# Kernel tuning notes

Hardware: AMD Instinct MI355X
Metric: run time of the kernel (lower is better)

Reference implementation:

```python
import jax, jax.numpy as jnp
import numpy as np

N_NODES = 50000
N_EDGES = 800000
IN_CH = 256
HID = 64
HEADS = 4
NEG_SLOPE = 0.2  # PyG GATConv default


def setup_inputs() -> dict:
    key = jax.random.key(0)
    ks = jax.random.split(key, 12)
    glorot = lambda k, shape: jax.random.normal(k, shape, jnp.float32) * (2.0 / (shape[0] + shape[-1])) ** 0.5
    d1 = HEADS * HID  # 256: width after conv1 (concat heads)
    return {
        "x": jax.random.normal(ks[0], (N_NODES, IN_CH), jnp.float32),
        "edge_index": jax.random.randint(ks[1], (2, N_EDGES), 0, N_NODES, jnp.int64),
        # conv1: GATConv(IN_CH, HID, heads=HEADS)
        "W1": glorot(ks[2], (IN_CH, HEADS * HID)),
        "a_src1": glorot(ks[3], (HEADS, HID)),
        "a_dst1": glorot(ks[4], (HEADS, HID)),
        "b1": jnp.zeros((HEADS * HID,), jnp.float32),
        # conv2: GATConv(d1, d1, heads=1)
        "W2": glorot(ks[5], (d1, d1)),
        "a_src2": glorot(ks[6], (1, d1)),
        "a_dst2": glorot(ks[7], (1, d1)),
        "b2": jnp.zeros((d1,), jnp.float32),
    }


def gat_conv(x, src, dst, W, a_src, a_dst, b, heads, out_ch, n_nodes):
    """PyG-style GATConv: per-head linear, additive attention, segment softmax over dst."""
    h = (x @ W).reshape(n_nodes, heads, out_ch)            # [N, H, C]
    alpha_src = jnp.sum(h * a_src, axis=-1)                # [N, H]
    alpha_dst = jnp.sum(h * a_dst, axis=-1)                # [N, H]
    e = jax.nn.leaky_relu(alpha_src[src] + alpha_dst[dst], NEG_SLOPE)  # [E, H]
    # numerically-stable segment softmax grouped by destination node
    e_max = jax.ops.segment_max(e, dst, num_segments=n_nodes)         # [N, H]
    e_exp = jnp.exp(e - e_max[dst])
    denom = jax.ops.segment_sum(e_exp, dst, num_segments=n_nodes)
    alpha = e_exp / denom[dst]                                        # [E, H]
    out = jax.ops.segment_sum(alpha[:, :, None] * h[src], dst, num_segments=n_nodes)  # [N, H, C]
    return out.reshape(n_nodes, heads * out_ch) + b


def reference(x, edge_index, W1, a_src1, a_dst1, b1, W2, a_src2, a_dst2, b2):
    n = x.shape[0]
    loops = jnp.arange(n, dtype=edge_index.dtype)
    src = jnp.concatenate([edge_index[0], loops])  # add self-loops (PyG default)
    dst = jnp.concatenate([edge_index[1], loops])
    h1 = gat_conv(x, src, dst, W1, a_src1, a_dst1, b1, HEADS, HID, n)
    h1 = jax.nn.elu(h1)
    out = gat_conv(h1, src, dst, W2, a_src2, a_dst2, b2, 1, HEADS * HID, n)
    return out
```

## Files before the change

kernel.cpp:

```cpp
#include <hip/hip_runtime.h>
#include <stdint.h>

typedef __bf16 bfv8 __attribute__((ext_vector_type(8)));
typedef float f32x4 __attribute__((ext_vector_type(4)));

__device__ __forceinline__ float b2f(unsigned short u) {
    union { unsigned int i; float f; } v; v.i = ((unsigned int)u) << 16; return v.f;
}
__device__ __forceinline__ unsigned short f2b(float f) {
    unsigned int x = __float_as_uint(f);
    unsigned int r = x + 0x7FFFu + ((x >> 16) & 1u);
    return (unsigned short)(r >> 16);
}
__device__ __forceinline__ float squash(float v) {
    return (v == v && fabsf(v) < 1e30f) ? v : 0.f;
}
__device__ __forceinline__ float blo(unsigned int w) {
    union { unsigned int i; float f; } v; v.i = w << 16; return v.f;
}
__device__ __forceinline__ float bhi(unsigned int w) {
    union { unsigned int i; float f; } v; v.i = w & 0xffff0000u; return v.f;
}

__device__ __forceinline__ void detect_reg(const void* x, const void* ei, int& f32w, int& i64w) {
    const unsigned short* xu = (const unsigned short*)x;
    const int* e32 = (const int*)ei;
    int bad = 0, oz = 0;
#pragma unroll
    for (int j = 0; j < 64; j++) {
        float v = b2f(xu[j]);
        if (!(fabsf(v) < 1e10f)) bad++;
    }
#pragma unroll
    for (int j = 1; j < 16; j += 2)
        if (e32[j] == 0) oz++;
    f32w = (bad >= 2) ? 1 : 0;
    i64w = (oz >= 6) ? 1 : 0;
}

__device__ __forceinline__ int edge_at(const void* ei, int idx, int i64) {
    return i64 ? (int)(((const long long*)ei)[idx]) : ((const int*)ei)[idx];
}

__global__ __launch_bounds__(256) void k_prep(
        const void* __restrict__ x, const void* __restrict__ ei,
        const void* __restrict__ W1, const void* __restrict__ W2,
        const void* __restrict__ a_src1, const void* __restrict__ a_dst1, const void* __restrict__ b1,
        const void* __restrict__ a_src2, const void* __restrict__ a_dst2, const void* __restrict__ b2,
        unsigned short* __restrict__ xb, unsigned short* __restrict__ WT1,
        unsigned short* __restrict__ WT2, unsigned short* __restrict__ vecs,
        int* __restrict__ deg, int* __restrict__ flags,
        int E, int ET, int N, int total8, int nconv, int nhist) {
    __shared__ unsigned short t[32][33];
    int f32w, i64w;
    detect_reg(x, ei, f32w, i64w);
    int b = blockIdx.x;
    int tid = threadIdx.x;

    if (b < nconv) {
        int i = b * 256 + tid;
        if (i >= total8) return;
        if (f32w) {
            const float4* f = (const float4*)x;
            float4 a = f[2 * i], bb = f[2 * i + 1];
            uint4 o;
            o.x = (unsigned)f2b(squash(a.x)) | ((unsigned)f2b(squash(a.y)) << 16);
            o.y = (unsigned)f2b(squash(a.z)) | ((unsigned)f2b(squash(a.w)) << 16);
            o.z = (unsigned)f2b(squash(bb.x)) | ((unsigned)f2b(squash(bb.y)) << 16);
            o.w = (unsigned)f2b(squash(bb.z)) | ((unsigned)f2b(squash(bb.w)) << 16);
            *(uint4*)(xb + 8 * (size_t)i) = o;
        } else {
            *(uint4*)(xb + 8 * (size_t)i) = ((const uint4*)x)[i];
        }
    } else if (b < nconv + 128) {
        int tb2 = b - nconv;
        const void* W = (tb2 < 64) ? W1 : W2;
        unsigned short* WT = (tb2 < 64) ? WT1 : WT2;
        int t6 = tb2 & 63;
        int bx = (t6 & 7) * 32, by = (t6 >> 3) * 32;
        int tx = tid & 31, ty = tid >> 5;
        for (int j = 0; j < 32; j += 8) {
            size_t idx = (size_t)(by + ty + j) * 256 + bx + tx;
            t[ty + j][tx] = f32w ? f2b(squash(((const float*)W)[idx]))
                                 : ((const unsigned short*)W)[idx];
        }
        __syncthreads();
        for (int j = 0; j < 32; j += 8)
            WT[(size_t)(bx + ty + j) * 256 + by + tx] = t[tx][ty + j];
    } else if (b < nconv + 128 + nhist) {
        int i = (b - nconv - 128) * 256 + tid;
        if (i >= ET) return;
        int d = (i < E) ? edge_at(ei, E + i, i64w) : (i - E);
        d = min(max(d, 0), N - 1);
        atomicAdd(&deg[d], 1);
    } else {
        const void* ptrs[6] = {a_src1, a_dst1, b1, a_src2, a_dst2, b2};
#pragma unroll
        for (int j = 0; j < 6; j++) {
            unsigned short u = f32w ? f2b(squash(((const float*)ptrs[j])[tid]))
                                    : ((const unsigned short*)ptrs[j])[tid];
            vecs[j * 256 + tid] = u;
        }
        if (tid == 0) { flags[0] = f32w; flags[1] = i64w; }
    }
}

__global__ __launch_bounds__(256) void k_csr(const int* __restrict__ deg,
        int* __restrict__ row_start, int* __restrict__ cursor,
        unsigned short* __restrict__ csr16, int* __restrict__ fz,
        int N, int ET) {
    __shared__ int sm[256];
    __shared__ int s_prefix;
    const int b = blockIdx.x, tid = threadIdx.x;
    const int i = b * 256 + tid;
    int v = (i < N) ? deg[i] : 0;
    sm[tid] = v; __syncthreads();
    for (int off = 1; off < 256; off <<= 1) {
        int t = (tid >= off) ? sm[tid - off] : 0;
        __syncthreads();
        sm[tid] += t;
        __syncthreads();
    }
    int incl = sm[tid];
    int total = sm[255];
    if (tid == 0) {
        int val = (b == 0) ? ((total << 2) | 2) : ((total << 2) | 1);
        __threadfence();
        atomicExch(&fz[b], val);
    }
    if (b == 0) {
        if (tid == 0) s_prefix = 0;
    } else if (tid < 64) {
        int prefix = 0, base = b - 1, done = 0;
        while (!done) {
            int p = base - tid;
            int val;
            if (p >= 0) {
                do { val = atomicAdd(&fz[p], 0); } while (val == 0);
            } else {
                val = 2;
            }
            unsigned long long im = __ballot((val & 2) != 0);
            int fi = (int)__ffsll(im) - 1;
            int mv = val >> 2;
            int contrib = (fi < 0 || tid <= fi) ? mv : 0;
            for (int o = 1; o < 64; o <<= 1) contrib += __shfl_xor(contrib, o, 64);
            prefix += contrib;
            if (fi >= 0) done = 1; else base -= 64;
        }
        if (tid == 0) {
            s_prefix = prefix;
            __threadfence();
            atomicExch(&fz[b], ((prefix + total) << 2) | 2);
        }
    }
    __syncthreads();
    int pre = s_prefix;
    if (i < N) {
        int rs = pre + incl - v;
        row_start[i] = rs;
        cursor[i] = rs;
    }
    if (b == 0 && tid == 0) row_start[N] = ET;
    if (b == 0 && tid < 64) csr16[ET + tid] = 0;
}

__global__ void k_scatter(const void* __restrict__ ei, int* __restrict__ cursor,
                          unsigned short* __restrict__ csr16, const int* __restrict__ flags,
                          int E, int ET, int N) {
    int i = blockIdx.x * 256 + threadIdx.x;
    if (i >= ET) return;
    int s, d;
    if (i < E) {
        int i64 = flags[1];
        s = edge_at(ei, i, i64);
        d = edge_at(ei, E + i, i64);
    } else {
        s = i - E; d = i - E;
    }
    s = min(max(s, 0), N - 1);
    d = min(max(d, 0), N - 1);
    int pos = atomicAdd(&cursor[d], 1);
    pos = min(max(pos, 0), ET - 1);
    csr16[pos] = (unsigned short)s;
}

__global__ __launch_bounds__(256) void k_gemm(const unsigned short* __restrict__ A,
                                              const unsigned short* __restrict__ BT,
                                              unsigned short* __restrict__ C,
                                              const unsigned short* __restrict__ avs,
                                              const unsigned short* __restrict__ avd,
                                              float* __restrict__ as_out,
                                              float* __restrict__ ad_out, int M) {
    __shared__ __align__(16) unsigned short As[128 * 72];
    __shared__ __align__(16) unsigned short Bs[128 * 72];
    const int tid = threadIdx.x;
    const int m0 = blockIdx.x * 128, n0 = blockIdx.y * 128;
    const int w = tid >> 6, lane = tid & 63;
    const int wm = (w & 1) * 64, wn = (w >> 1) * 64;
    const int lr = lane & 15, lk = (lane >> 4) * 8;
    const int sr = tid >> 1, sc = (tid & 1) * 32;

    f32x4 acc[4][4];
#pragma unroll
    for (int a = 0; a < 4; a++)
#pragma unroll
        for (int b = 0; b < 4; b++) acc[a][b] = (f32x4){0.f, 0.f, 0.f, 0.f};

    for (int k0 = 0; k0 < 256; k0 += 64) {
        uint4 va0, va1, va2, va3;
        if (m0 + sr < M) {
            const uint4* Ap = (const uint4*)(A + (size_t)(m0 + sr) * 256 + k0 + sc);
            va0 = Ap[0]; va1 = Ap[1]; va2 = Ap[2]; va3 = Ap[3];
        } else {
            va0 = va1 = va2 = va3 = make_uint4(0, 0, 0, 0);
        }
        {
            uint4* Ad = (uint4*)&As[sr * 72 + sc];
            Ad[0] = va0; Ad[1] = va1; Ad[2] = va2; Ad[3] = va3;
        }
        {
            const uint4* Bp = (const uint4*)(BT + (size_t)(n0 + sr) * 256 + k0 + sc);
            uint4* Bd = (uint4*)&Bs[sr * 72 + sc];
            Bd[0] = Bp[0]; Bd[1] = Bp[1]; Bd[2] = Bp[2]; Bd[3] = Bp[3];
        }
        __syncthreads();
#pragma unroll
        for (int kk = 0; kk < 64; kk += 32) {
            bfv8 af[4], bfr[4];
#pragma unroll
            for (int mi = 0; mi < 4; mi++)
                af[mi] = *(const bfv8*)&As[(wm + mi * 16 + lr) * 72 + kk + lk];
#pragma unroll
            for (int ni = 0; ni < 4; ni++)
                bfr[ni] = *(const bfv8*)&Bs[(wn + ni * 16 + lr) * 72 + kk + lk];
#pragma unroll
            for (int mi = 0; mi < 4; mi++)
#pragma unroll
                for (int ni = 0; ni < 4; ni++)
                    acc[mi][ni] = __builtin_amdgcn_mfma_f32_16x16x32_bf16(af[mi], bfr[ni], acc[mi][ni], 0, 0, 0);
        }
        __syncthreads();
    }
    const int rb = (lane >> 4) * 4;
#pragma unroll
    for (int mi = 0; mi < 4; mi++) {
#pragma unroll
        for (int r = 0; r < 4; r++) {
            int row = m0 + wm + mi * 16 + rb + r;
            if (row < M) {
#pragma unroll
                for (int ni = 0; ni < 4; ni++)
                    C[(size_t)row * 256 + n0 + wn + ni * 16 + lr] = f2b(squash(acc[mi][ni][r]));
            }
        }
    }
    const int slice = (n0 + wn) >> 6;
    float asl[4], adl[4];
#pragma unroll
    for (int ni = 0; ni < 4; ni++) {
        int col = n0 + wn + ni * 16 + lr;
        asl[ni] = b2f(avs[col]);
        adl[ni] = b2f(avd[col]);
    }
#pragma unroll
    for (int mi = 0; mi < 4; mi++) {
#pragma unroll
        for (int r = 0; r < 4; r++) {
            float ps = 0.f, pd = 0.f;
#pragma unroll
            for (int ni = 0; ni < 4; ni++) {
                float cv = acc[mi][ni][r];
                ps = fmaf(cv, asl[ni], ps);
                pd = fmaf(cv, adl[ni], pd);
            }
#pragma unroll
            for (int off = 1; off < 16; off <<= 1) {
                ps += __shfl_xor(ps, off, 64);
                pd += __shfl_xor(pd, off, 64);
            }
            int row = m0 + wm + mi * 16 + rb + r;
            if (lr == 0 && row < M) {
                as_out[(size_t)row * 4 + slice] = squash(ps);
                ad_out[(size_t)row * 4 + slice] = squash(pd);
            }
        }
    }
}

#define AGG_ISSUE(eb, hv)                                                     \
    {                                                                         \
        _Pragma("unroll") for (int u = 0; u < 8; u++) {                       \
            const int e = (eb) * 8 + u;                                       \
            unsigned o = __shfl(off, (lw & 32) + e, 64);                      \
            uint4 z = make_uint4(0, 0, 0, 0);                                 \
            hv[u] = (e < cnt) ? *(const uint4*)(Hb + (size_t)o + lb) : z;     \
        }                                                                     \
    }
#define AGG_CONSUME(eb, hv)                                                   \
    if ((eb) * 8 < cnt) {                                                     \
        _Pragma("unroll") for (int u = 0; u < 8; u++) {                       \
            const int e = (eb) * 8 + u;                                       \
            float wj = wbase[e * 4];                                          \
            a0 = fmaf(wj, blo(hv[u].x), a0); a1 = fmaf(wj, bhi(hv[u].x), a1); \
            a2 = fmaf(wj, blo(hv[u].y), a2); a3 = fmaf(wj, bhi(hv[u].y), a3); \
            a4 = fmaf(wj, blo(hv[u].z), a4); a5 = fmaf(wj, bhi(hv[u].z), a5); \
            a6 = fmaf(wj, blo(hv[u].w), a6); a7 = fmaf(wj, bhi(hv[u].w), a7); \
        }                                                                     \
    }

template <int H>
__global__ __launch_bounds__(256) void k_agg(
        const unsigned short* __restrict__ Hm, const float* __restrict__ asrc,
        const float* __restrict__ adst, const int* __restrict__ row_start,
        const unsigned short* __restrict__ csr16, const unsigned short* __restrict__ bias,
        void* __restrict__ out, const int* __restrict__ flags,
        int N, int ET, int elu, int is_final) {
    __shared__ __align__(16) float lwv[8][32][4];
    const int tid = threadIdx.x;
    const int hw = tid >> 5;
    const int l = tid & 31;
    const int lw = tid & 63;
    const int node = blockIdx.x * 8 + hw;
    if (node >= N) return;
    const int h = (l * H) >> 5;
    const int lb = l * 16;
    int rs = row_start[node], re = row_start[node + 1];
    rs = min(max(rs, 0), ET);
    re = min(max(re, rs), ET);

    float adnx = 0.f, adny = 0.f, adnz = 0.f, adnw = 0.f;
    {
        float4 t = *(const float4*)(adst + (size_t)node * 4);
        if (H == 4) { adnx = t.x; adny = t.y; adnz = t.z; adnw = t.w; }
        else        { adnx = t.x + t.y + t.z + t.w; }
    }

    float lsx = 0.f, lsy = 0.f, lsz = 0.f, lsw = 0.f;
    float a0 = 0.f, a1 = 0.f, a2 = 0.f, a3 = 0.f, a4 = 0.f, a5 = 0.f, a6 = 0.f, a7 = 0.f;
    const float* wbase = &lwv[hw][0][0] + h;
    const char* Hb = (const char*)Hm;

    for (int c = rs; c < re; c += 32) {
        const int cnt = min(32, re - c);
        float4 w4 = make_float4(0.f, 0.f, 0.f, 0.f);
        unsigned int off = 0;
        int idx = 0;
        const bool act = (l < cnt);
        if (act) idx = min((int)csr16[c + l], N - 1);
        off = (unsigned)idx << 9;

        uint4 hvA[8], hvB[8];
        AGG_ISSUE(0, hvA);
        if (8 < cnt) AGG_ISSUE(1, hvB);

        if (act) {
            float4 av = *(const float4*)(asrc + (size_t)idx * 4);
            if (H == 4) {
                float ex = av.x + adnx, ey = av.y + adny;
                float ez = av.z + adnz, ew = av.w + adnw;
                ex = (ex < 0.f) ? 0.2f * ex : ex;
                ey = (ey < 0.f) ? 0.2f * ey : ey;
                ez = (ez < 0.f) ? 0.2f * ez : ez;
                ew = (ew < 0.f) ? 0.2f * ew : ew;
                w4.x = __expf(fminf(ex, 80.f)); w4.y = __expf(fminf(ey, 80.f));
                w4.z = __expf(fminf(ez, 80.f)); w4.w = __expf(fminf(ew, 80.f));
            } else {
                float ev = (av.x + av.y + av.z + av.w) + adnx;
                ev = (ev < 0.f) ? 0.2f * ev : ev;
                w4.x = __expf(fminf(ev, 80.f));
            }
        }
        lsx += w4.x;
        if (H == 4) { lsy += w4.y; lsz += w4.z; lsw += w4.w; }
        *(float4*)&lwv[hw][l][0] = w4;
        asm volatile("s_waitcnt lgkmcnt(0)");

        AGG_CONSUME(0, hvA);
        if (16 < cnt) AGG_ISSUE(2, hvA);
        AGG_CONSUME(1, hvB);
        if (24 < cnt) AGG_ISSUE(3, hvB);
        AGG_CONSUME(2, hvA);
        AGG_CONSUME(3, hvB);
    }

    for (int off = 1; off < 32; off <<= 1) {
        lsx += __shfl_xor(lsx, off, 64);
        if (H == 4) {
            lsy += __shfl_xor(lsy, off, 64);
            lsz += __shfl_xor(lsz, off, 64);
            lsw += __shfl_xor(lsw, off, 64);
        }
    }
    float ls = (H == 4) ? ((h == 0) ? lsx : (h == 1) ? lsy : (h == 2) ? lsz : lsw) : lsx;
    float inv = (ls > 0.f) ? 1.f / ls : 0.f;

    const int cc = 8 * l;
    uint4 bv = *(const uint4*)(bias + cc);
    float o0 = a0 * inv + blo(bv.x), o1 = a1 * inv + bhi(bv.x);
    float o2 = a2 * inv + blo(bv.y), o3 = a3 * inv + bhi(bv.y);
    float o4 = a4 * inv + blo(bv.z), o5 = a5 * inv + bhi(bv.z);
    float o6 = a6 * inv + blo(bv.w), o7 = a7 * inv + bhi(bv.w);
    if (elu) {
        o0 = (o0 > 0.f) ? o0 : __expf(o0) - 1.f;
        o1 = (o1 > 0.f) ? o1 : __expf(o1) - 1.f;
        o2 = (o2 > 0.f) ? o2 : __expf(o2) - 1.f;
        o3 = (o3 > 0.f) ? o3 : __expf(o3) - 1.f;
        o4 = (o4 > 0.f) ? o4 : __expf(o4) - 1.f;
        o5 = (o5 > 0.f) ? o5 : __expf(o5) - 1.f;
        o6 = (o6 > 0.f) ? o6 : __expf(o6) - 1.f;
        o7 = (o7 > 0.f) ? o7 : __expf(o7) - 1.f;
    }
    o0 = squash(o0); o1 = squash(o1); o2 = squash(o2); o3 = squash(o3);
    o4 = squash(o4); o5 = squash(o5); o6 = squash(o6); o7 = squash(o7);
    if (is_final && flags[0]) {
        float* op = (float*)out + (size_t)node * 256 + cc;
        *(float4*)op       = make_float4(o0, o1, o2, o3);
        *(float4*)(op + 4) = make_float4(o4, o5, o6, o7);
    } else {
        uint4 ov;
        ov.x = (unsigned)f2b(o0) | ((unsigned)f2b(o1) << 16);
        ov.y = (unsigned)f2b(o2) | ((unsigned)f2b(o3) << 16);
        ov.z = (unsigned)f2b(o4) | ((unsigned)f2b(o5) << 16);
        ov.w = (unsigned)f2b(o6) | ((unsigned)f2b(o7) << 16);
        *(uint4*)((unsigned short*)out + (size_t)node * 256 + cc) = ov;
    }
}

extern "C" void kernel_launch(void* const* d_in, const int* in_sizes, int n_in,
                              void* d_out, int out_size, void* d_ws, size_t ws_size,
                              hipStream_t stream) {
    const void* x      = d_in[0];
    const void* ei     = d_in[1];
    const void* W1     = d_in[2];
    const void* a_src1 = d_in[3];
    const void* a_dst1 = d_in[4];
    const void* b1     = d_in[5];
    const void* W2     = d_in[6];
    const void* a_src2 = d_in[7];
    const void* a_dst2 = d_in[8];
    const void* b2     = d_in[9];

    const int N  = in_sizes[0] / 256;
    const int E  = in_sizes[1] / 2;
    const int ET = E + N;

    char* p = (char*)d_ws;
    auto alloc = [&](size_t bytes) -> char* {
        char* r = p;
        p += (bytes + 255) & ~(size_t)255;
        return r;
    };
    int* flags = (int*)alloc(256);
    unsigned short* WT1  = (unsigned short*)alloc(256 * 256 * 2);
    unsigned short* WT2  = (unsigned short*)alloc(256 * 256 * 2);
    unsigned short* vecs = (unsigned short*)alloc(6 * 256 * 2);
    float* as_ = (float*)alloc((size_t)N * 4 * 4);
    float* ad_ = (float*)alloc((size_t)N * 4 * 4);
    int* deg   = (int*)alloc((size_t)N * 4);
    int* fz    = (int*)alloc(1024);
    int* row_start = (int*)alloc((size_t)(N + 1) * 4);
    int* cursor    = (int*)alloc((size_t)N * 4);
    unsigned short* csr16 = (unsigned short*)alloc((size_t)(ET + 64) * 2);

    unsigned short* BUF_OUT = (unsigned short*)d_out;
    unsigned short* BUF_IN0 = (unsigned short*)d_in[0];

    const size_t degpad = ((size_t)N * 4 + 255) & ~(size_t)255;
    hipMemsetAsync(deg, 0, degpad + 1024, stream);

    const int total8 = N * 256 / 8;
    const int nconv  = (total8 + 255) / 256;
    const int nhist  = (ET + 255) / 256;
    const int nprep  = nconv + 128 + nhist + 1;

    k_prep<<<nprep, 256, 0, stream>>>(x, ei, W1, W2, a_src1, a_dst1, b1, a_src2, a_dst2, b2,
                                      BUF_OUT, WT1, WT2, vecs, deg, flags,
                                      E, ET, N, total8, nconv, nhist);

    int nb = (N + 255) / 256;
    k_csr<<<nb, 256, 0, stream>>>(deg, row_start, cursor, csr16, fz, N, ET);
    k_scatter<<<nhist, 256, 0, stream>>>(ei, cursor, csr16, flags, E, ET, N);

    int gm = (N + 127) / 128;
    int ab = (N + 7) / 8;

    k_gemm<<<dim3(gm, 2), 256, 0, stream>>>(BUF_OUT, WT1, BUF_IN0,
                                            vecs + 0 * 256, vecs + 1 * 256, as_, ad_, N);
    k_agg<4><<<ab, 256, 0, stream>>>(BUF_IN0, as_, ad_, row_start, csr16, vecs + 2 * 256,
                                     BUF_OUT, flags, N, ET, 1, 0);
    k_gemm<<<dim3(gm, 2), 256, 0, stream>>>(BUF_OUT, WT2, BUF_IN0,
                                            vecs + 3 * 256, vecs + 4 * 256, as_, ad_, N);
    k_agg<1><<<ab, 256, 0, stream>>>(BUF_IN0, as_, ad_, row_start, csr16, vecs + 5 * 256,
                                     d_out, flags, N, ET, 0, 1);
}
```

Before: 467.8 us.

## Split aggregation into denominator pass and column-sliced gather kernel

Replaces the single fused aggregation kernel with two kernels. The first computes per-node softmax denominators. The second splits the 256 feature columns into 8 slices across blocks, with 16 lanes per node each gathering 4 bytes per neighbor row. The split is meant to shrink each block's gather footprint and register use so more waves can be resident. In exchange, each edge's index and attention logit are read and recomputed 8 times, every row gather becomes a narrow 4-byte access, and there is an extra launch and pass over the CSR.

```diff
diff --git a/kernel.cpp b/kernel.cpp
--- a/kernel.cpp
+++ b/kernel.cpp
@@ -288,43 +288,15 @@
     }
 }
 
-#define AGG_ISSUE(eb, hv)                                                     \
-    {                                                                         \
-        _Pragma("unroll") for (int u = 0; u < 8; u++) {                       \
-            const int e = (eb) * 8 + u;                                       \
-            unsigned o = __shfl(off, (lw & 32) + e, 64);                      \
-            uint4 z = make_uint4(0, 0, 0, 0);                                 \
-            hv[u] = (e < cnt) ? *(const uint4*)(Hb + (size_t)o + lb) : z;     \
-        }                                                                     \
-    }
-#define AGG_CONSUME(eb, hv)                                                   \
-    if ((eb) * 8 < cnt) {                                                     \
-        _Pragma("unroll") for (int u = 0; u < 8; u++) {                       \
-            const int e = (eb) * 8 + u;                                       \
-            float wj = wbase[e * 4];                                          \
-            a0 = fmaf(wj, blo(hv[u].x), a0); a1 = fmaf(wj, bhi(hv[u].x), a1); \
-            a2 = fmaf(wj, blo(hv[u].y), a2); a3 = fmaf(wj, bhi(hv[u].y), a3); \
-            a4 = fmaf(wj, blo(hv[u].z), a4); a5 = fmaf(wj, bhi(hv[u].z), a5); \
-            a6 = fmaf(wj, blo(hv[u].w), a6); a7 = fmaf(wj, bhi(hv[u].w), a7); \
-        }                                                                     \
-    }
-
 template <int H>
-__global__ __launch_bounds__(256) void k_agg(
-        const unsigned short* __restrict__ Hm, const float* __restrict__ asrc,
-        const float* __restrict__ adst, const int* __restrict__ row_start,
-        const unsigned short* __restrict__ csr16, const unsigned short* __restrict__ bias,
-        void* __restrict__ out, const int* __restrict__ flags,
-        int N, int ET, int elu, int is_final) {
-    __shared__ __align__(16) float lwv[8][32][4];
+__global__ __launch_bounds__(256) void k_denom(
+        const float* __restrict__ asrc, const float* __restrict__ adst,
+        const int* __restrict__ row_start, const unsigned short* __restrict__ csr16,
+        float* __restrict__ invd, int N, int ET) {
     const int tid = threadIdx.x;
-    const int hw = tid >> 5;
-    const int l = tid & 31;
-    const int lw = tid & 63;
+    const int hw = tid >> 5, l = tid & 31;
     const int node = blockIdx.x * 8 + hw;
     if (node >= N) return;
-    const int h = (l * H) >> 5;
-    const int lb = l * 16;
     int rs = row_start[node], re = row_start[node + 1];
     rs = min(max(rs, 0), ET);
     re = min(max(re, rs), ET);
@@ -335,55 +307,25 @@
         if (H == 4) { adnx = t.x; adny = t.y; adnz = t.z; adnw = t.w; }
         else        { adnx = t.x + t.y + t.z + t.w; }
     }
-
     float lsx = 0.f, lsy = 0.f, lsz = 0.f, lsw = 0.f;
-    float a0 = 0.f, a1 = 0.f, a2 = 0.f, a3 = 0.f, a4 = 0.f, a5 = 0.f, a6 = 0.f, a7 = 0.f;
-    const float* wbase = &lwv[hw][0][0] + h;
-    const char* Hb = (const char*)Hm;
-
-    for (int c = rs; c < re; c += 32) {
-        const int cnt = min(32, re - c);
-        float4 w4 = make_float4(0.f, 0.f, 0.f, 0.f);
-        unsigned int off = 0;
-        int idx = 0;
-        const bool act = (l < cnt);
-        if (act) idx = min((int)csr16[c + l], N - 1);
-        off = (unsigned)idx << 9;
-
-        uint4 hvA[8], hvB[8];
-        AGG_ISSUE(0, hvA);
-        if (8 < cnt) AGG_ISSUE(1, hvB);
-
-        if (act) {
-            float4 av = *(const float4*)(asrc + (size_t)idx * 4);
-            if (H == 4) {
-                float ex = av.x + adnx, ey = av.y + adny;
-                float ez = av.z + adnz, ew = av.w + adnw;
-                ex = (ex < 0.f) ? 0.2f * ex : ex;
-                ey = (ey < 0.f) ? 0.2f * ey : ey;
-                ez = (ez < 0.f) ? 0.2f * ez : ez;
-                ew = (ew < 0.f) ? 0.2f * ew : ew;
-                w4.x = __expf(fminf(ex, 80.f)); w4.y = __expf(fminf(ey, 80.f));
-                w4.z = __expf(fminf(ez, 80.f)); w4.w = __expf(fminf(ew, 80.f));
-            } else {
-                float ev = (av.x + av.y + av.z + av.w) + adnx;
-                ev = (ev < 0.f) ? 0.2f * ev : ev;
-                w4.x = __expf(fminf(ev, 80.f));
-            }
-        }
-        lsx += w4.x;
-        if (H == 4) { lsy += w4.y; lsz += w4.z; lsw += w4.w; }
-        *(float4*)&lwv[hw][l][0] = w4;
-        asm volatile("s_waitcnt lgkmcnt(0)");
-
-        AGG_CONSUME(0, hvA);
-        if (16 < cnt) AGG_ISSUE(2, hvA);
-        AGG_CONSUME(1, hvB);
-        if (24 < cnt) AGG_ISSUE(3, hvB);
-        AGG_CONSUME(2, hvA);
-        AGG_CONSUME(3, hvB);
-    }
-
+    for (int c = rs + l; c < re; c += 32) {
+        int idx = min((int)csr16[c], N - 1);
+        float4 av = *(const float4*)(asrc + (size_t)idx * 4);
+        if (H == 4) {
+            float ex = av.x + adnx, ey = av.y + adny;
+            float ez = av.z + adnz, ew = av.w + adnw;
+            ex = (ex < 0.f) ? 0.2f * ex : ex;
+            ey = (ey < 0.f) ? 0.2f * ey : ey;
+            ez = (ez < 0.f) ? 0.2f * ez : ez;
+            ew = (ew < 0.f) ? 0.2f * ew : ew;
+            lsx += __expf(fminf(ex, 80.f)); lsy += __expf(fminf(ey, 80.f));
+            lsz += __expf(fminf(ez, 80.f)); lsw += __expf(fminf(ew, 80.f));
+        } else {
+            float ev = (av.x + av.y + av.z + av.w) + adnx;
+            ev = (ev < 0.f) ? 0.2f * ev : ev;
+            lsx += __expf(fminf(ev, 80.f));
+        }
+    }
     for (int off = 1; off < 32; off <<= 1) {
         lsx += __shfl_xor(lsx, off, 64);
         if (H == 4) {
@@ -392,38 +334,92 @@
             lsw += __shfl_xor(lsw, off, 64);
         }
     }
-    float ls = (H == 4) ? ((h == 0) ? lsx : (h == 1) ? lsy : (h == 2) ? lsz : lsw) : lsx;
-    float inv = (ls > 0.f) ? 1.f / ls : 0.f;
-
-    const int cc = 8 * l;
-    uint4 bv = *(const uint4*)(bias + cc);
-    float o0 = a0 * inv + blo(bv.x), o1 = a1 * inv + bhi(bv.x);
-    float o2 = a2 * inv + blo(bv.y), o3 = a3 * inv + bhi(bv.y);
-    float o4 = a4 * inv + blo(bv.z), o5 = a5 * inv + bhi(bv.z);
-    float o6 = a6 * inv + blo(bv.w), o7 = a7 * inv + bhi(bv.w);
+    if (l == 0) {
+        float4 iv;
+        iv.x = (lsx > 0.f) ? 1.f / lsx : 0.f;
+        iv.y = (H == 4 && lsy > 0.f) ? 1.f / lsy : 0.f;
+        iv.z = (H == 4 && lsz > 0.f) ? 1.f / lsz : 0.f;
+        iv.w = (H == 4 && lsw > 0.f) ? 1.f / lsw : 0.f;
+        *(float4*)(invd + (size_t)node * 4) = iv;
+    }
+}
+
+template <int H>
+__global__ __launch_bounds__(256) void k_aggs(
+        const unsigned short* __restrict__ Hm, const float* __restrict__ asrc,
+        const float* __restrict__ adst, const float* __restrict__ invd,
+        const int* __restrict__ row_start, const unsigned short* __restrict__ csr16,
+        const unsigned short* __restrict__ bias, void* __restrict__ out,
+        const int* __restrict__ flags, int N, int ET, int elu, int is_final) {
+    const int tid = threadIdx.x;
+    const int s = blockIdx.x & 7;
+    const int g = tid >> 4;
+    const int gl = tid & 15;
+    const int node = (blockIdx.x >> 3) * 16 + g;
+    if (node >= N) return;
+    const int h = (H == 4) ? (s >> 1) : 0;
+    const unsigned rowoff = (unsigned)(s * 64 + gl * 4);
+    int rs = row_start[node], re = row_start[node + 1];
+    rs = min(max(rs, 0), ET);
+    re = min(max(re, rs), ET);
+
+    float adn;
+    if (H == 4) {
+        adn = adst[(size_t)node * 4 + h];
+    } else {
+        float4 t = *(const float4*)(adst + (size_t)node * 4);
+        adn = t.x + t.y + t.z + t.w;
+    }
+    const float inv = invd[(size_t)node * 4 + h];
+    const char* Hb = (const char*)Hm;
+
+    float acc0 = 0.f, acc1 = 0.f;
+    for (int c = rs; c < re; c += 8) {
+        const int cnt = min(8, re - c);
+        int idx[8];
+        unsigned hv[8];
+        float wj[8];
+#pragma unroll
+        for (int u = 0; u < 8; u++)
+            idx[u] = min((int)csr16[c + u], N - 1);
+#pragma unroll
+        for (int u = 0; u < 8; u++)
+            hv[u] = *(const unsigned*)(Hb + ((size_t)idx[u] << 9) + rowoff);
+#pragma unroll
+        for (int u = 0; u < 8; u++) {
+            float e;
+            if (H == 4) {
+                e = asrc[(size_t)idx[u] * 4 + h] + adn;
+            } else {
+                float4 t = *(const float4*)(asrc + (size_t)idx[u] * 4);
+                e = (t.x + t.y + t.z + t.w) + adn;
+            }
+            e = (e < 0.f) ? 0.2f * e : e;
+            float ww = __expf(fminf(e, 80.f)) * inv;
+            wj[u] = (u < cnt) ? ww : 0.f;
+        }
+#pragma unroll
+        for (int u = 0; u < 8; u++) {
+            acc0 = fmaf(wj[u], blo(hv[u]), acc0);
+            acc1 = fmaf(wj[u], bhi(hv[u]), acc1);
+        }
+    }
+
+    unsigned bv = *(const unsigned*)((const char*)bias + rowoff);
+    float o0 = acc0 + blo(bv);
+    float o1 = acc1 + bhi(bv);
     if (elu) {
         o0 = (o0 > 0.f) ? o0 : __expf(o0) - 1.f;
         o1 = (o1 > 0.f) ? o1 : __expf(o1) - 1.f;
-        o2 = (o2 > 0.f) ? o2 : __expf(o2) - 1.f;
-        o3 = (o3 > 0.f) ? o3 : __expf(o3) - 1.f;
-        o4 = (o4 > 0.f) ? o4 : __expf(o4) - 1.f;
-        o5 = (o5 > 0.f) ? o5 : __expf(o5) - 1.f;
-        o6 = (o6 > 0.f) ? o6 : __expf(o6) - 1.f;
-        o7 = (o7 > 0.f) ? o7 : __expf(o7) - 1.f;
-    }
-    o0 = squash(o0); o1 = squash(o1); o2 = squash(o2); o3 = squash(o3);
-    o4 = squash(o4); o5 = squash(o5); o6 = squash(o6); o7 = squash(o7);
+    }
+    o0 = squash(o0); o1 = squash(o1);
+    const int col = s * 32 + gl * 2;
     if (is_final && flags[0]) {
-        float* op = (float*)out + (size_t)node * 256 + cc;
-        *(float4*)op       = make_float4(o0, o1, o2, o3);
-        *(float4*)(op + 4) = make_float4(o4, o5, o6, o7);
+        float2 ov; ov.x = o0; ov.y = o1;
+        *(float2*)((float*)out + (size_t)node * 256 + col) = ov;
     } else {
-        uint4 ov;
-        ov.x = (unsigned)f2b(o0) | ((unsigned)f2b(o1) << 16);
-        ov.y = (unsigned)f2b(o2) | ((unsigned)f2b(o3) << 16);
-        ov.z = (unsigned)f2b(o4) | ((unsigned)f2b(o5) << 16);
-        ov.w = (unsigned)f2b(o6) | ((unsigned)f2b(o7) << 16);
-        *(uint4*)((unsigned short*)out + (size_t)node * 256 + cc) = ov;
+        unsigned ov = (unsigned)f2b(o0) | ((unsigned)f2b(o1) << 16);
+        *(unsigned*)((unsigned short*)out + (size_t)node * 256 + col) = ov;
     }
 }
 
@@ -455,8 +451,9 @@
     unsigned short* WT1  = (unsigned short*)alloc(256 * 256 * 2);
     unsigned short* WT2  = (unsigned short*)alloc(256 * 256 * 2);
     unsigned short* vecs = (unsigned short*)alloc(6 * 256 * 2);
-    float* as_ = (float*)alloc((size_t)N * 4 * 4);
-    float* ad_ = (float*)alloc((size_t)N * 4 * 4);
+    float* as_  = (float*)alloc((size_t)N * 4 * 4);
+    float* ad_  = (float*)alloc((size_t)N * 4 * 4);
+    float* invd = (float*)alloc((size_t)N * 4 * 4);
     int* deg   = (int*)alloc((size_t)N * 4);
     int* fz    = (int*)alloc(1024);
     int* row_start = (int*)alloc((size_t)(N + 1) * 4);
@@ -482,15 +479,18 @@
     k_csr<<<nb, 256, 0, stream>>>(deg, row_start, cursor, csr16, fz, N, ET);
     k_scatter<<<nhist, 256, 0, stream>>>(ei, cursor, csr16, flags, E, ET, N);
 
-    int gm = (N + 127) / 128;
-    int ab = (N + 7) / 8;
+    int gm  = (N + 127) / 128;
+    int db  = (N + 7) / 8;
+    int ab2 = ((N + 15) / 16) * 8;
 
     k_gemm<<<dim3(gm, 2), 256, 0, stream>>>(BUF_OUT, WT1, BUF_IN0,
                                             vecs + 0 * 256, vecs + 1 * 256, as_, ad_, N);
-    k_agg<4><<<ab, 256, 0, stream>>>(BUF_IN0, as_, ad_, row_start, csr16, vecs + 2 * 256,
-                                     BUF_OUT, flags, N, ET, 1, 0);
+    k_denom<4><<<db, 256, 0, stream>>>(as_, ad_, row_start, csr16, invd, N, ET);
+    k_aggs<4><<<ab2, 256, 0, stream>>>(BUF_IN0, as_, ad_, invd, row_start, csr16,
+                                       vecs + 2 * 256, BUF_OUT, flags, N, ET, 1, 0);
     k_gemm<<<dim3(gm, 2), 256, 0, stream>>>(BUF_OUT, WT2, BUF_IN0,
                                             vecs + 3 * 256, vecs + 4 * 256, as_, ad_, N);
-    k_agg<1><<<ab, 256, 0, stream>>>(BUF_IN0, as_, ad_, row_start, csr16, vecs + 5 * 256,
-                                     d_out, flags, N, ET, 0, 1);
-}
+    k_denom<1><<<db, 256, 0, stream>>>(as_, ad_, row_start, csr16, invd, N, ET);
+    k_aggs<1><<<ab2, 256, 0, stream>>>(BUF_IN0, as_, ad_, invd, row_start, csr16,
+                                       vecs + 5 * 256, d_out, flags, N, ET, 0, 1);
+}
```

Result: slower. 528.4 us (+13.0%).

## Use grid-stride persistent aggregation with LDS neighbor offsets and simpler gather loop

Applied to the files above, without the earlier changes.

The aggregation kernel now caps the grid at 2048 blocks, and each half-wave loops over destination nodes in grid-stride fashion instead of handling exactly one node. Neighbor row offsets are now passed through shared memory rather than shuffles. The gathers are no longer issued early, before the attention exponentials are computed; the loop instead handles fixed batches of 8 with a separate tail batch. This aims to cut block launch overhead and improve load balance, but it drops the overlap between the feature gathers and the exp computation.

```diff
diff --git a/kernel.cpp b/kernel.cpp
--- a/kernel.cpp
+++ b/kernel.cpp
@@ -288,27 +288,6 @@
     }
 }
 
-#define AGG_ISSUE(eb, hv)                                                     \
-    {                                                                         \
-        _Pragma("unroll") for (int u = 0; u < 8; u++) {                       \
-            const int e = (eb) * 8 + u;                                       \
-            unsigned o = __shfl(off, (lw & 32) + e, 64);                      \
-            uint4 z = make_uint4(0, 0, 0, 0);                                 \
-            hv[u] = (e < cnt) ? *(const uint4*)(Hb + (size_t)o + lb) : z;     \
-        }                                                                     \
-    }
-#define AGG_CONSUME(eb, hv)                                                   \
-    if ((eb) * 8 < cnt) {                                                     \
-        _Pragma("unroll") for (int u = 0; u < 8; u++) {                       \
-            const int e = (eb) * 8 + u;                                       \
-            float wj = wbase[e * 4];                                          \
-            a0 = fmaf(wj, blo(hv[u].x), a0); a1 = fmaf(wj, bhi(hv[u].x), a1); \
-            a2 = fmaf(wj, blo(hv[u].y), a2); a3 = fmaf(wj, bhi(hv[u].y), a3); \
-            a4 = fmaf(wj, blo(hv[u].z), a4); a5 = fmaf(wj, bhi(hv[u].z), a5); \
-            a6 = fmaf(wj, blo(hv[u].w), a6); a7 = fmaf(wj, bhi(hv[u].w), a7); \
-        }                                                                     \
-    }
-
 template <int H>
 __global__ __launch_bounds__(256) void k_agg(
         const unsigned short* __restrict__ Hm, const float* __restrict__ asrc,
@@ -317,113 +296,146 @@
         void* __restrict__ out, const int* __restrict__ flags,
         int N, int ET, int elu, int is_final) {
     __shared__ __align__(16) float lwv[8][32][4];
+    __shared__ unsigned int loff[8][32];
     const int tid = threadIdx.x;
     const int hw = tid >> 5;
     const int l = tid & 31;
-    const int lw = tid & 63;
-    const int node = blockIdx.x * 8 + hw;
-    if (node >= N) return;
     const int h = (l * H) >> 5;
     const int lb = l * 16;
-    int rs = row_start[node], re = row_start[node + 1];
-    rs = min(max(rs, 0), ET);
-    re = min(max(re, rs), ET);
-
-    float adnx = 0.f, adny = 0.f, adnz = 0.f, adnw = 0.f;
-    {
-        float4 t = *(const float4*)(adst + (size_t)node * 4);
-        if (H == 4) { adnx = t.x; adny = t.y; adnz = t.z; adnw = t.w; }
-        else        { adnx = t.x + t.y + t.z + t.w; }
-    }
-
-    float lsx = 0.f, lsy = 0.f, lsz = 0.f, lsw = 0.f;
-    float a0 = 0.f, a1 = 0.f, a2 = 0.f, a3 = 0.f, a4 = 0.f, a5 = 0.f, a6 = 0.f, a7 = 0.f;
     const float* wbase = &lwv[hw][0][0] + h;
+    const unsigned int* obase = &loff[hw][0];
     const char* Hb = (const char*)Hm;
-
-    for (int c = rs; c < re; c += 32) {
-        const int cnt = min(32, re - c);
-        float4 w4 = make_float4(0.f, 0.f, 0.f, 0.f);
-        unsigned int off = 0;
-        int idx = 0;
-        const bool act = (l < cnt);
-        if (act) idx = min((int)csr16[c + l], N - 1);
-        off = (unsigned)idx << 9;
-
-        uint4 hvA[8], hvB[8];
-        AGG_ISSUE(0, hvA);
-        if (8 < cnt) AGG_ISSUE(1, hvB);
-
-        if (act) {
-            float4 av = *(const float4*)(asrc + (size_t)idx * 4);
+    const int stride = gridDim.x * 8;
+
+    for (int node = blockIdx.x * 8 + hw; node < N; node += stride) {
+        int rs = row_start[node], re = row_start[node + 1];
+        rs = min(max(rs, 0), ET);
+        re = min(max(re, rs), ET);
+
+        float adnx = 0.f, adny = 0.f, adnz = 0.f, adnw = 0.f;
+        {
+            float4 t = *(const float4*)(adst + (size_t)node * 4);
+            if (H == 4) { adnx = t.x; adny = t.y; adnz = t.z; adnw = t.w; }
+            else        { adnx = t.x + t.y + t.z + t.w; }
+        }
+
+        float lsx = 0.f, lsy = 0.f, lsz = 0.f, lsw = 0.f;
+        float a0 = 0.f, a1 = 0.f, a2 = 0.f, a3 = 0.f;
+        float a4 = 0.f, a5 = 0.f, a6 = 0.f, a7 = 0.f;
+
+        for (int c = rs; c < re; c += 32) {
+            const int cnt = min(32, re - c);
+            float4 w4 = make_float4(0.f, 0.f, 0.f, 0.f);
+            unsigned int off = 0;
+            if (l < cnt) {
+                int idx = min((int)csr16[c + l], N - 1);
+                off = (unsigned)idx << 9;
+                float4 av = *(const float4*)(asrc + (size_t)idx * 4);
+                if (H == 4) {
+                    float ex = av.x + adnx, ey = av.y + adny;
+                    float ez = av.z + adnz, ew = av.w + adnw;
+                    ex = (ex < 0.f) ? 0.2f * ex : ex;
+                    ey = (ey < 0.f) ? 0.2f * ey : ey;
+                    ez = (ez < 0.f) ? 0.2f * ez : ez;
+                    ew = (ew < 0.f) ? 0.2f * ew : ew;
+                    w4.x = __expf(fminf(ex, 80.f)); w4.y = __expf(fminf(ey, 80.f));
+                    w4.z = __expf(fminf(ez, 80.f)); w4.w = __expf(fminf(ew, 80.f));
+                } else {
+                    float ev = (av.x + av.y + av.z + av.w) + adnx;
+                    ev = (ev < 0.f) ? 0.2f * ev : ev;
+                    w4.x = __expf(fminf(ev, 80.f));
+                }
+            }
+            lsx += w4.x;
+            if (H == 4) { lsy += w4.y; lsz += w4.z; lsw += w4.w; }
+            *(float4*)&lwv[hw][l][0] = w4;
+            loff[hw][l] = off;
+            asm volatile("s_waitcnt lgkmcnt(0)");
+
+            const int full = cnt & ~7;
+            int jb = 0;
+            for (; jb < full; jb += 8) {
+                unsigned int o_[8];
+                uint4 hv[8];
+                float wj[8];
+#pragma unroll
+                for (int u = 0; u < 8; u++) o_[u] = obase[jb + u];
+#pragma unroll
+                for (int u = 0; u < 8; u++) hv[u] = *(const uint4*)(Hb + (size_t)o_[u] + lb);
+#pragma unroll
+                for (int u = 0; u < 8; u++) wj[u] = wbase[(jb + u) * 4];
+#pragma unroll
+                for (int u = 0; u < 8; u++) {
+                    a0 = fmaf(wj[u], blo(hv[u].x), a0); a1 = fmaf(wj[u], bhi(hv[u].x), a1);
+                    a2 = fmaf(wj[u], blo(hv[u].y), a2); a3 = fmaf(wj[u], bhi(hv[u].y), a3);
+                    a4 = fmaf(wj[u], blo(hv[u].z), a4); a5 = fmaf(wj[u], bhi(hv[u].z), a5);
+                    a6 = fmaf(wj[u], blo(hv[u].w), a6); a7 = fmaf(wj[u], bhi(hv[u].w), a7);
+                }
+            }
+            if (jb < cnt) {
+                const int rem = cnt - jb;
+                unsigned int o_[8];
+                uint4 hv[8];
+                float wj[8];
+#pragma unroll
+                for (int u = 0; u < 8; u++) o_[u] = obase[jb + u];
+#pragma unroll
+                for (int u = 0; u < 8; u++) {
+                    uint4 z = make_uint4(0, 0, 0, 0);
+                    hv[u] = (u < rem) ? *(const uint4*)(Hb + (size_t)o_[u] + lb) : z;
+                }
+#pragma unroll
+                for (int u = 0; u < 8; u++) wj[u] = wbase[(jb + u) * 4];
+#pragma unroll
+                for (int u = 0; u < 8; u++) {
+                    a0 = fmaf(wj[u], blo(hv[u].x), a0); a1 = fmaf(wj[u], bhi(hv[u].x), a1);
+                    a2 = fmaf(wj[u], blo(hv[u].y), a2); a3 = fmaf(wj[u], bhi(hv[u].y), a3);
+                    a4 = fmaf(wj[u], blo(hv[u].z), a4); a5 = fmaf(wj[u], bhi(hv[u].z), a5);
+                    a6 = fmaf(wj[u], blo(hv[u].w), a6); a7 = fmaf(wj[u], bhi(hv[u].w), a7);
+                }
+            }
+        }
+        for (int off = 1; off < 32; off <<= 1) {
+            lsx += __shfl_xor(lsx, off, 64);
             if (H == 4) {
-                float ex = av.x + adnx, ey = av.y + adny;
-                float ez = av.z + adnz, ew = av.w + adnw;
-                ex = (ex < 0.f) ? 0.2f * ex : ex;
-                ey = (ey < 0.f) ? 0.2f * ey : ey;
-                ez = (ez < 0.f) ? 0.2f * ez : ez;
-                ew = (ew < 0.f) ? 0.2f * ew : ew;
-                w4.x = __expf(fminf(ex, 80.f)); w4.y = __expf(fminf(ey, 80.f));
-                w4.z = __expf(fminf(ez, 80.f)); w4.w = __expf(fminf(ew, 80.f));
-            } else {
-                float ev = (av.x + av.y + av.z + av.w) + adnx;
-                ev = (ev < 0.f) ? 0.2f * ev : ev;
-                w4.x = __expf(fminf(ev, 80.f));
-            }
-        }
-        lsx += w4.x;
-        if (H == 4) { lsy += w4.y; lsz += w4.z; lsw += w4.w; }
-        *(float4*)&lwv[hw][l][0] = w4;
-        asm volatile("s_waitcnt lgkmcnt(0)");
-
-        AGG_CONSUME(0, hvA);
-        if (16 < cnt) AGG_ISSUE(2, hvA);
-        AGG_CONSUME(1, hvB);
-        if (24 < cnt) AGG_ISSUE(3, hvB);
-        AGG_CONSUME(2, hvA);
-        AGG_CONSUME(3, hvB);
-    }
-
-    for (int off = 1; off < 32; off <<= 1) {
-        lsx += __shfl_xor(lsx, off, 64);
-        if (H == 4) {
-            lsy += __shfl_xor(lsy, off, 64);
-            lsz += __shfl_xor(lsz, off, 64);
-            lsw += __shfl_xor(lsw, off, 64);
-        }
-    }
-    float ls = (H == 4) ? ((h == 0) ? lsx : (h == 1) ? lsy : (h == 2) ? lsz : lsw) : lsx;
-    float inv = (ls > 0.f) ? 1.f / ls : 0.f;
-
-    const int cc = 8 * l;
-    uint4 bv = *(const uint4*)(bias + cc);
-    float o0 = a0 * inv + blo(bv.x), o1 = a1 * inv + bhi(bv.x);
-    float o2 = a2 * inv + blo(bv.y), o3 = a3 * inv + bhi(bv.y);
-    float o4 = a4 * inv + blo(bv.z), o5 = a5 * inv + bhi(bv.z);
-    float o6 = a6 * inv + blo(bv.w), o7 = a7 * inv + bhi(bv.w);
-    if (elu) {
-        o0 = (o0 > 0.f) ? o0 : __expf(o0) - 1.f;
-        o1 = (o1 > 0.f) ? o1 : __expf(o1) - 1.f;
-        o2 = (o2 > 0.f) ? o2 : __expf(o2) - 1.f;
-        o3 = (o3 > 0.f) ? o3 : __expf(o3) - 1.f;
-        o4 = (o4 > 0.f) ? o4 : __expf(o4) - 1.f;
-        o5 = (o5 > 0.f) ? o5 : __expf(o5) - 1.f;
-        o6 = (o6 > 0.f) ? o6 : __expf(o6) - 1.f;
-        o7 = (o7 > 0.f) ? o7 : __expf(o7) - 1.f;
-    }
-    o0 = squash(o0); o1 = squash(o1); o2 = squash(o2); o3 = squash(o3);
-    o4 = squash(o4); o5 = squash(o5); o6 = squash(o6); o7 = squash(o7);
-    if (is_final && flags[0]) {
-        float* op = (float*)out + (size_t)node * 256 + cc;
-        *(float4*)op       = make_float4(o0, o1, o2, o3);
-        *(float4*)(op + 4) = make_float4(o4, o5, o6, o7);
-    } else {
-        uint4 ov;
-        ov.x = (unsigned)f2b(o0) | ((unsigned)f2b(o1) << 16);
-        ov.y = (unsigned)f2b(o2) | ((unsigned)f2b(o3) << 16);
-        ov.z = (unsigned)f2b(o4) | ((unsigned)f2b(o5) << 16);
-        ov.w = (unsigned)f2b(o6) | ((unsigned)f2b(o7) << 16);
-        *(uint4*)((unsigned short*)out + (size_t)node * 256 + cc) = ov;
+                lsy += __shfl_xor(lsy, off, 64);
+                lsz += __shfl_xor(lsz, off, 64);
+                lsw += __shfl_xor(lsw, off, 64);
+            }
+        }
+        float ls = (H == 4) ? ((h == 0) ? lsx : (h == 1) ? lsy : (h == 2) ? lsz : lsw) : lsx;
+        float inv = (ls > 0.f) ? 1.f / ls : 0.f;
+
+        const int cc = 8 * l;
+        uint4 bv = *(const uint4*)(bias + cc);
+        float o0 = a0 * inv + blo(bv.x), o1 = a1 * inv + bhi(bv.x);
+        float o2 = a2 * inv + blo(bv.y), o3 = a3 * inv + bhi(bv.y);
+        float o4 = a4 * inv + blo(bv.z), o5 = a5 * inv + bhi(bv.z);
+        float o6 = a6 * inv + blo(bv.w), o7 = a7 * inv + bhi(bv.w);
+        if (elu) {
+            o0 = (o0 > 0.f) ? o0 : __expf(o0) - 1.f;
+            o1 = (o1 > 0.f) ? o1 : __expf(o1) - 1.f;
+            o2 = (o2 > 0.f) ? o2 : __expf(o2) - 1.f;
+            o3 = (o3 > 0.f) ? o3 : __expf(o3) - 1.f;
+            o4 = (o4 > 0.f) ? o4 : __expf(o4) - 1.f;
+            o5 = (o5 > 0.f) ? o5 : __expf(o5) - 1.f;
+            o6 = (o6 > 0.f) ? o6 : __expf(o6) - 1.f;
+            o7 = (o7 > 0.f) ? o7 : __expf(o7) - 1.f;
+        }
+        o0 = squash(o0); o1 = squash(o1); o2 = squash(o2); o3 = squash(o3);
+        o4 = squash(o4); o5 = squash(o5); o6 = squash(o6); o7 = squash(o7);
+        if (is_final && flags[0]) {
+            float* op = (float*)out + (size_t)node * 256 + cc;
+            *(float4*)op       = make_float4(o0, o1, o2, o3);
+            *(float4*)(op + 4) = make_float4(o4, o5, o6, o7);
+        } else {
+            uint4 ov;
+            ov.x = (unsigned)f2b(o0) | ((unsigned)f2b(o1) << 16);
+            ov.y = (unsigned)f2b(o2) | ((unsigned)f2b(o3) << 16);
+            ov.z = (unsigned)f2b(o4) | ((unsigned)f2b(o5) << 16);
+            ov.w = (unsigned)f2b(o6) | ((unsigned)f2b(o7) << 16);
+            *(uint4*)((unsigned short*)out + (size_t)node * 256 + cc) = ov;
+        }
     }
 }
 
@@ -484,6 +496,7 @@
 
     int gm = (N + 127) / 128;
     int ab = (N + 7) / 8;
+    if (ab > 2048) ab = 2048;
 
     k_gemm<<<dim3(gm, 2), 256, 0, stream>>>(BUF_OUT, WT1, BUF_IN0,
                                             vecs + 0 * 256, vecs + 1 * 256, as_, ad_, N);
```

Measured after the change: 404.0 us. -13.6%, faster.
